# Kernel optimization log

Measured on AMD Instinct MI355X. Metric: run time of the kernel, lower is better.

## Reference

```python
import jax, jax.numpy as jnp
import numpy as np

N_JOINTS = 16
N_VERTS = 778
# standard MANO kinematic tree (parent of joint i; root parent is -1, unused)
PARENTS = np.array([-1, 0, 1, 2, 0, 4, 5, 0, 7, 8, 0, 10, 11, 0, 13, 14])
# rotate_base=True: root rotation is post-multiplied by 180-deg rotation about x
ROT_X = np.array([[1.0, 0.0, 0.0], [0.0, -1.0, 0.0], [0.0, 0.0, -1.0]], dtype=np.float32)


def _batch_rodrigues(theta):
    # theta: [M, 3] axis-angle -> [M, 3, 3] rotation matrices (via quaternion, HMR-style)
    angle = jnp.linalg.norm(theta + 1e-8, axis=1, keepdims=True)
    axis = theta / angle
    half = 0.5 * angle
    quat = jnp.concatenate([jnp.cos(half), jnp.sin(half) * axis], axis=1)
    quat = quat / jnp.linalg.norm(quat, axis=1, keepdims=True)
    w, x, y, z = quat[:, 0], quat[:, 1], quat[:, 2], quat[:, 3]
    w2, x2, y2, z2 = w * w, x * x, y * y, z * z
    wx, wy, wz = w * x, w * y, w * z
    xy, xz, yz = x * y, x * z, y * z
    R = jnp.stack([
        w2 + x2 - y2 - z2, 2 * xy - 2 * wz, 2 * wy + 2 * xz,
        2 * wz + 2 * xy, w2 - x2 + y2 - z2, 2 * yz - 2 * wx,
        2 * xz - 2 * wy, 2 * wx + 2 * yz, w2 - x2 - y2 + z2,
    ], axis=1)
    return R.reshape(-1, 3, 3)


def _make_A(R, t):
    # R: [N,3,3], t: [N,3] -> [N,4,4] homogeneous transform
    top = jnp.concatenate([R, t[:, :, None]], axis=2)          # [N,3,4]
    bot = jnp.broadcast_to(jnp.array([0.0, 0.0, 0.0, 1.0], R.dtype), (R.shape[0], 1, 4))
    return jnp.concatenate([top, bot], axis=1)


def _global_rigid_transform(Rs, J):
    # Rs: [N,16,3,3], J: [N,16,3]
    root_rotation = jnp.matmul(Rs[:, 0], jnp.asarray(ROT_X, Rs.dtype))
    results = [_make_A(root_rotation, J[:, 0])]
    for i in range(1, N_JOINTS):
        p = int(PARENTS[i])
        t = J[:, i] - J[:, p]
        results.append(jnp.matmul(results[p], _make_A(Rs[:, i], t)))
    G = jnp.stack(results, axis=1)                              # [N,16,4,4]
    J_transformed = G[:, :, :3, 3]
    # A = G - pad(G[:, :, :3, :3] @ J) : remove joint-rest translation
    rel = jnp.einsum('njab,njb->nja', G[:, :, :3, :3], J)       # [N,16,3]
    A = G.at[:, :, :3, 3].add(-rel)
    return J_transformed, A


def setup_inputs() -> dict:
    key = jax.random.key(0)
    ks = jax.random.split(key, 7)
    N = 4096
    return {
        'beta': jax.random.normal(ks[0], (N, 10), jnp.float32),
        'theta': jax.random.normal(ks[1], (N, 48), jnp.float32) * 0.3,
        'v_template': jax.random.normal(ks[2], (N_VERTS, 3), jnp.float32) * 0.1,
        'shapedirs': jax.random.normal(ks[3], (10, N_VERTS * 3), jnp.float32) * 0.01,
        'J_regressor': jax.random.uniform(ks[4], (N_VERTS, N_JOINTS), jnp.float32) / N_VERTS,
        'posedirs': jax.random.normal(ks[5], (135, N_VERTS * 3), jnp.float32) * 0.01,
        'weights': jax.random.uniform(ks[6], (N_VERTS, N_JOINTS), jnp.float32),
    }


def reference(beta, theta, v_template, shapedirs, J_regressor, posedirs, weights):
    N = beta.shape[0]
    # shape blendshapes
    v_shaped = jnp.matmul(beta, shapedirs).reshape(N, N_VERTS, 3) + v_template
    # rest joints from vertices
    J = jnp.einsum('nvc,vj->njc', v_shaped, J_regressor)        # [N,16,3]
    # pose rotations
    Rs = _batch_rodrigues(theta.reshape(-1, 3)).reshape(N, N_JOINTS, 3, 3)
    # pose blendshapes (exclude root)
    pose_feature = (Rs[:, 1:] - jnp.eye(3, dtype=Rs.dtype)).reshape(N, 135)
    v_posed = jnp.matmul(pose_feature, posedirs).reshape(N, N_VERTS, 3) + v_shaped
    # kinematic chain
    J_transformed, A = _global_rigid_transform(Rs, J)
    # linear blend skinning
    T = jnp.einsum('vj,njab->nvab', weights, A)                 # [N,778,4,4]
    ones = jnp.ones((N, N_VERTS, 1), v_posed.dtype)
    v_homo = jnp.concatenate([v_posed, ones], axis=2)           # [N,778,4]
    verts = jnp.einsum('nvab,nvb->nva', T, v_homo)[:, :, :3]    # [N,778,3]
    joints = jnp.einsum('nvc,vj->njc', verts, J_regressor)      # [N,16,3]
    return verts, joints, Rs
```

## Files before the change

kernel.cpp:

```cpp
#include <hip/hip_runtime.h>
#include <math.h>

#define NJ 16
#define NV 778
#define M3 2334
#define NTB 156

typedef float f32x4  __attribute__((ext_vector_type(4)));
typedef float f32x16 __attribute__((ext_vector_type(16)));
typedef short bf16x8 __attribute__((ext_vector_type(8)));

__device__ __forceinline__ unsigned short f2bf(float x) {
    unsigned int u = __float_as_uint(x);
    unsigned int r = (u + 0x7FFF + ((u >> 16) & 1)) >> 16;
    return (unsigned short)r;
}


__global__ __launch_bounds__(256, 1) void k01_prep(
    const float* __restrict__ shapedirs,
    const float* __restrict__ posedirs,
    const float* __restrict__ Jreg,
    const float* __restrict__ vtemp,
    const float* __restrict__ theta,
    float* __restrict__ SJJT,
    float* __restrict__ RsOut,
    bf16x8* __restrict__ Bf,
    int N)
{
    const int tid = threadIdx.x;
    const int rodBlocks = (N * NJ) / 256;
    if (blockIdx.x < 44) {
        int task = blockIdx.x * 4 + (tid >> 6);
        int lane = tid & 63;
        if (task < 176) {
            int b = task >> 4;
            int j = task & 15;
            const float* src = (b < 10) ? (shapedirs + (size_t)b * M3) : vtemp;
            float a0 = 0.f, a1 = 0.f, a2 = 0.f;
            for (int v = lane; v < NV; v += 64) {
                float jr = Jreg[v * 16 + j];
                a0 = fmaf(src[v*3 + 0], jr, a0);
                a1 = fmaf(src[v*3 + 1], jr, a1);
                a2 = fmaf(src[v*3 + 2], jr, a2);
            }
#pragma unroll
            for (int m = 1; m < 64; m <<= 1) {
                a0 += __shfl_xor(a0, m);
                a1 += __shfl_xor(a1, m);
                a2 += __shfl_xor(a2, m);
            }
            if (lane == 0) {
                int base = (b < 10) ? (b*48 + j*3) : (480 + j*3);
                SJJT[base + 0] = a0;
                SJJT[base + 1] = a1;
                SJJT[base + 2] = a2;
            }
        }
        return;
    }
    if (blockIdx.x < 44 + rodBlocks) {
        int idx = (blockIdx.x - 44) * 256 + tid;
        int n = idx >> 4;
        int j = idx & 15;
        float t0 = theta[n*48 + j*3 + 0];
        float t1 = theta[n*48 + j*3 + 1];
        float t2 = theta[n*48 + j*3 + 2];
        const float eps = 1e-8f;
        float a0 = t0 + eps, a1 = t1 + eps, a2 = t2 + eps;
        float angle = sqrtf(a0*a0 + a1*a1 + a2*a2);
        float inv  = 1.0f / angle;
        float half = 0.5f * angle;
        float sh = sinf(half), chh = cosf(half);
        float qw = chh;
        float qx = sh * t0 * inv;
        float qy = sh * t1 * inv;
        float qz = sh * t2 * inv;
        float qn = 1.0f / sqrtf(qw*qw + qx*qx + qy*qy + qz*qz);
        qw *= qn; qx *= qn; qy *= qn; qz *= qn;
        float w2=qw*qw, x2=qx*qx, y2=qy*qy, z2=qz*qz;
        float wx=qw*qx, wy=qw*qy, wz=qw*qz;
        float xy=qx*qy, xz=qx*qz, yz=qy*qz;
        float* R = RsOut + (size_t)idx * 9;
        R[0] = w2 + x2 - y2 - z2;
        R[1] = 2.f*(xy - wz);
        R[2] = 2.f*(wy + xz);
        R[3] = 2.f*(wz + xy);
        R[4] = w2 - x2 + y2 - z2;
        R[5] = 2.f*(yz - wx);
        R[6] = 2.f*(xz - wy);
        R[7] = 2.f*(wx + yz);
        R[8] = w2 - x2 - y2 + z2;
        return;
    }
    int idx = (blockIdx.x - 44 - rodBlocks) * 256 + tid;
    int nB = NTB * 5 * 64;
    if (idx >= nB) return;
    int lane = idx & 63;
    int ks   = (idx >> 6) % 5;
    int nt   = idx / 320;
    int col = nt * 16 + (lane & 15);
    int k0  = ks * 32 + (lane >> 4) * 8;
    bf16x8 o;
#pragma unroll
    for (int j = 0; j < 8; ++j) {
        int k = k0 + j;
        float val = 0.f;
        if (col < M3) {
            if (k < 10)       val = shapedirs[(size_t)k * M3 + col];
            else if (k < 145) val = posedirs[(size_t)(k - 10) * M3 + col];
        }
        o[j] = (short)f2bf(val);
    }
    Bf[idx] = o;
}

__global__ __launch_bounds__(256, 1) void k2m(
    const float* __restrict__ beta,
    const float* __restrict__ Rs,
    const float* __restrict__ SJJT,
    float* __restrict__ Aws,
    bf16x8* __restrict__ Af,
    int N)
{
    const int tid = threadIdx.x;
    const int KB2 = (N * 5 + 255) / 256;
    if (blockIdx.x < KB2) {
        __shared__ float sS[528];
        for (int i = tid; i < 528; i += 256) sS[i] = SJJT[i];
        __syncthreads();
        int gid = blockIdx.x * 256 + tid;
        if (gid >= N * 5) return;
        int n  = gid / 5;
        int ch = gid % 5;

        float b[10];
#pragma unroll
        for (int i = 0; i < 10; ++i) b[i] = beta[n*10 + i];

        int jidx[4];
        jidx[0] = 0; jidx[1] = ch*3 + 1; jidx[2] = ch*3 + 2; jidx[3] = ch*3 + 3;
        float J[4][3];
#pragma unroll
        for (int q = 0; q < 4; ++q) {
            int j = jidx[q];
#pragma unroll
            for (int c = 0; c < 3; ++c) {
                float acc = sS[480 + j*3 + c];
#pragma unroll
                for (int qq = 0; qq < 10; ++qq)
                    acc = fmaf(b[qq], sS[qq*48 + j*3 + c], acc);
                J[q][c] = acc;
            }
        }

        const float* Rn = Rs + (size_t)n * 144;
        float* An = Aws + (size_t)n * 192;

        float GpR[9], Gpt[3];
#pragma unroll
        for (int r = 0; r < 3; ++r) {
            GpR[r*3+0] =  Rn[r*3+0];
            GpR[r*3+1] = -Rn[r*3+1];
            GpR[r*3+2] = -Rn[r*3+2];
        }
        Gpt[0] = J[0][0]; Gpt[1] = J[0][1]; Gpt[2] = J[0][2];

        if (ch == 0) {
#pragma unroll
            for (int r = 0; r < 3; ++r) {
                float rel = GpR[r*3+0]*J[0][0] + GpR[r*3+1]*J[0][1] + GpR[r*3+2]*J[0][2];
                An[r*4 + 0] = GpR[r*3+0];
                An[r*4 + 1] = GpR[r*3+1];
                An[r*4 + 2] = GpR[r*3+2];
                An[r*4 + 3] = Gpt[r] - rel;
            }
        }

#pragma unroll
        for (int st = 0; st < 3; ++st) {
            int i = jidx[st+1];
            const float* Ri = Rn + (size_t)i * 9;
            float t0 = J[st+1][0] - J[st][0];
            float t1 = J[st+1][1] - J[st][1];
            float t2 = J[st+1][2] - J[st][2];
            float GR[9], Gt[3];
#pragma unroll
            for (int r = 0; r < 3; ++r) {
#pragma unroll
                for (int c = 0; c < 3; ++c)
                    GR[r*3+c] = GpR[r*3+0]*Ri[c] + GpR[r*3+1]*Ri[3+c] + GpR[r*3+2]*Ri[6+c];
                Gt[r] = GpR[r*3+0]*t0 + GpR[r*3+1]*t1 + GpR[r*3+2]*t2 + Gpt[r];
            }
#pragma unroll
            for (int r = 0; r < 3; ++r) {
                float rel = GR[r*3+0]*J[st+1][0] + GR[r*3+1]*J[st+1][1] + GR[r*3+2]*J[st+1][2];
                An[i*12 + r*4 + 0] = GR[r*3+0];
                An[i*12 + r*4 + 1] = GR[r*3+1];
                An[i*12 + r*4 + 2] = GR[r*3+2];
                An[i*12 + r*4 + 3] = Gt[r] - rel;
            }
#pragma unroll
            for (int r = 0; r < 9; ++r) GpR[r] = GR[r];
            Gpt[0] = Gt[0]; Gpt[1] = Gt[1]; Gpt[2] = Gt[2];
        }
        return;
    }

    int idx = (blockIdx.x - KB2) * 256 + tid;
    int nA = (N / 16) * 5 * 64;
    if (idx >= nA) return;
    int lane = idx & 63;
    int ks   = (idx >> 6) % 5;
    int mt   = idx / 320;
    int n  = mt * 16 + (lane & 15);
    int k0 = ks * 32 + (lane >> 4) * 8;
    bf16x8 o;
#pragma unroll
    for (int j = 0; j < 8; ++j) {
        int k = k0 + j;
        float val;
        if (k < 10) {
            val = beta[(size_t)n * 10 + k];
        } else if (k < 145) {
            int kk = k - 10;
            int rr = kk % 9;
            val = Rs[(size_t)n * 144 + 9 + kk];
            if ((rr & 3) == 0) val -= 1.f;
        } else {
            val = 0.f;
        }
        o[j] = (short)f2bf(val);
    }
    Af[idx] = o;
}

__global__ __launch_bounds__(256, 1) void k34_gemm_blend(
    const bf16x8* __restrict__ Af,
    const bf16x8* __restrict__ Bf,
    const float* __restrict__ vtemp,
    const float* __restrict__ Aws,
    const float* __restrict__ weights,
    float* __restrict__ verts,
    int N)
{
    __shared__ float sC[16][194];
    const int tid  = threadIdx.x;
    const int w    = tid >> 6;
    const int lane = tid & 63;
    const int mt   = blockIdx.x;
    const int ntb  = blockIdx.y * 12 + w * 3;

    f32x4 acc0 = {0.f,0.f,0.f,0.f};
    f32x4 acc1 = {0.f,0.f,0.f,0.f};
    f32x4 acc2 = {0.f,0.f,0.f,0.f};

    const bf16x8* Ab = Af + (size_t)mt * 5 * 64 + lane;
    const bf16x8* Bb = Bf + lane;

#pragma unroll
    for (int ks = 0; ks < 5; ++ks) {
        bf16x8 a  = Ab[ks * 64];
        bf16x8 b0 = Bb[((size_t)(ntb+0) * 5 + ks) * 64];
        bf16x8 b1 = Bb[((size_t)(ntb+1) * 5 + ks) * 64];
        bf16x8 b2 = Bb[((size_t)(ntb+2) * 5 + ks) * 64];
        acc0 = __builtin_amdgcn_mfma_f32_16x16x32_bf16(a, b0, acc0, 0, 0, 0);
        acc1 = __builtin_amdgcn_mfma_f32_16x16x32_bf16(a, b1, acc1, 0, 0, 0);
        acc2 = __builtin_amdgcn_mfma_f32_16x16x32_bf16(a, b2, acc2, 0, 0, 0);
    }

    {
        const int rl = (lane >> 4) * 4;
        const int cl = w * 48 + (lane & 15);
#pragma unroll
        for (int r = 0; r < 4; ++r) {
            sC[rl + r][cl +  0] = acc0[r];
            sC[rl + r][cl + 16] = acc1[r];
            sC[rl + r][cl + 32] = acc2[r];
        }
    }
    __syncthreads();

    const int vg = blockIdx.y * 64 + lane;
    const bool valid = vg < NV;
    const int cvg = valid ? vg : (NV - 1);

    f32x16 wv = *reinterpret_cast<const f32x16*>(&weights[(size_t)cvg * 16]);
    float vtx = vtemp[cvg*3 + 0];
    float vty = vtemp[cvg*3 + 1];
    float vtz = vtemp[cvg*3 + 2];

#pragma unroll
    for (int it = 0; it < 4; ++it) {
        const int nl = w * 4 + it;
        const int n  = __builtin_amdgcn_readfirstlane(mt * 16 + nl);
        const float* An = Aws + (size_t)n * 192;

        float px = sC[nl][lane*3 + 0] + vtx;
        float py = sC[nl][lane*3 + 1] + vty;
        float pz = sC[nl][lane*3 + 2] + vtz;

        float ox = 0.f, oy = 0.f, oz = 0.f;
#define BJF(j_) { \
        float a0=An[(j_)*12+0],  a1=An[(j_)*12+1],  a2 =An[(j_)*12+2],  a3 =An[(j_)*12+3]; \
        float a4=An[(j_)*12+4],  a5=An[(j_)*12+5],  a6 =An[(j_)*12+6],  a7 =An[(j_)*12+7]; \
        float a8=An[(j_)*12+8],  a9=An[(j_)*12+9],  a10=An[(j_)*12+10], a11=An[(j_)*12+11]; \
        float X = fmaf(a0,px, fmaf(a1,py, fmaf(a2,pz, a3))); \
        float Y = fmaf(a4,px, fmaf(a5,py, fmaf(a6,pz, a7))); \
        float Z = fmaf(a8,px, fmaf(a9,py, fmaf(a10,pz, a11))); \
        ox = fmaf(wv[j_], X, ox); oy = fmaf(wv[j_], Y, oy); oz = fmaf(wv[j_], Z, oz); }
        BJF(0)  BJF(1)  BJF(2)  BJF(3)  BJF(4)  BJF(5)  BJF(6)  BJF(7)
        BJF(8)  BJF(9)  BJF(10) BJF(11) BJF(12) BJF(13) BJF(14) BJF(15)
#undef BJF

        if (valid) {
            float* o = verts + (size_t)(mt*16 + nl) * M3 + (size_t)vg * 3;
            o[0] = ox; o[1] = oy; o[2] = oz;
        }
    }
}

__global__ __launch_bounds__(256, 1) void k4b_joints(
    const float* __restrict__ verts,
    const float* __restrict__ Jreg,
    float* __restrict__ joints,
    int N)
{
    __shared__ float part[4][4][48];
    const int tid = threadIdx.x;
    const int nl  = tid >> 6;
    const int sub = tid & 63;
    const int j   = sub & 15;
    const int c4  = sub >> 4;
    const int n   = blockIdx.x * 4 + nl;

    int vbeg = c4 * 195;
    int vend = vbeg + 195; if (vend > NV) vend = NV;

    const float* vp = verts + (size_t)n * M3;
    float a0 = 0.f, a1 = 0.f, a2 = 0.f;
#pragma unroll 4
    for (int v = vbeg; v < vend; ++v) {
        float jr = Jreg[(size_t)v * 16 + j];
        float x = vp[v*3 + 0], y = vp[v*3 + 1], z = vp[v*3 + 2];
        a0 = fmaf(jr, x, a0);
        a1 = fmaf(jr, y, a1);
        a2 = fmaf(jr, z, a2);
    }
    part[nl][c4][j*3+0] = a0;
    part[nl][c4][j*3+1] = a1;
    part[nl][c4][j*3+2] = a2;
    __syncthreads();

    if (tid < 192) {
        int nl2 = tid / 48;
        int r   = tid % 48;
        float s = part[nl2][0][r] + part[nl2][1][r] + part[nl2][2][r] + part[nl2][3][r];
        joints[(size_t)(blockIdx.x * 4 + nl2) * 48 + r] = s;
    }
}

extern "C" void kernel_launch(void* const* d_in, const int* in_sizes, int n_in,
                              void* d_out, int out_size, void* d_ws, size_t ws_size,
                              hipStream_t stream)
{
    const float* beta   = (const float*)d_in[0];
    const float* theta  = (const float*)d_in[1];
    const float* vtemp  = (const float*)d_in[2];
    const float* shaped = (const float*)d_in[3];
    const float* Jreg   = (const float*)d_in[4];
    const float* posed  = (const float*)d_in[5];
    const float* wts    = (const float*)d_in[6];
    float* out = (float*)d_out;
    const int N = in_sizes[0] / 10;

    float* verts  = out;
    float* joints = out + (size_t)N * M3;
    float* RsOut  = joints + (size_t)N * 48;
    float* Aws    = (float*)d_ws;
    float*  fbase = Aws + (size_t)N * 192;
    bf16x8* Af    = (bf16x8*)fbase;
    bf16x8* Bf    = (bf16x8*)(fbase + (size_t)(N/16)*5*64*4);

    const int nA = (N / 16) * 5 * 64;
    const int nB = NTB * 5 * 64;
    const int rodBlocks = (N * NJ) / 256;
    const int KB2 = (N * 5 + 255) / 256;

    k01_prep<<<44 + rodBlocks + (nB + 255)/256, 256, 0, stream>>>(
        shaped, posed, Jreg, vtemp, theta, joints, RsOut, Bf, N);
    k2m<<<KB2 + (nA + 255)/256, 256, 0, stream>>>(
        beta, RsOut, joints, Aws, Af, N);
    k34_gemm_blend<<<dim3(N/16, 13), 256, 0, stream>>>(
        Af, Bf, vtemp, Aws, wts, verts, N);
    k4b_joints<<<N/4, 256, 0, stream>>>(verts, Jreg, joints, N);
}
```

Before: 82.20 us.

## Fold k2m into prep and GEMM kernels, recomputing Rodrigues for A-fragment packing

Removes the separate k2m launch. The bf16 A-fragment packing moves into the prep kernel, which recomputes the Rodrigues rotations from theta instead of waiting for the Rs output. The per-sample kinematic chain moves into the start of the GEMM/blend kernel, where 80 threads per block compute the transforms into the workspace. This saves a launch and a global round-trip for A, but every y-block redundantly recomputes the chain for its 16 samples and delays the MFMA work until it finishes.

```diff
diff --git a/kernel.cpp b/kernel.cpp
--- a/kernel.cpp
+++ b/kernel.cpp
@@ -14,6 +14,37 @@
     unsigned int u = __float_as_uint(x);
     unsigned int r = (u + 0x7FFF + ((u >> 16) & 1)) >> 16;
     return (unsigned short)r;
+}
+
+__device__ __forceinline__ void rodrigues9(
+    float t0, float t1, float t2,
+    float& r0, float& r1, float& r2, float& r3, float& r4,
+    float& r5, float& r6, float& r7, float& r8)
+{
+    const float eps = 1e-8f;
+    float a0 = t0 + eps, a1 = t1 + eps, a2 = t2 + eps;
+    float angle = sqrtf(a0*a0 + a1*a1 + a2*a2);
+    float inv  = 1.0f / angle;
+    float half = 0.5f * angle;
+    float sh = sinf(half), chh = cosf(half);
+    float qw = chh;
+    float qx = sh * t0 * inv;
+    float qy = sh * t1 * inv;
+    float qz = sh * t2 * inv;
+    float qn = 1.0f / sqrtf(qw*qw + qx*qx + qy*qy + qz*qz);
+    qw *= qn; qx *= qn; qy *= qn; qz *= qn;
+    float w2=qw*qw, x2=qx*qx, y2=qy*qy, z2=qz*qz;
+    float wx=qw*qx, wy=qw*qy, wz=qw*qz;
+    float xy=qx*qy, xz=qx*qz, yz=qy*qz;
+    r0 = w2 + x2 - y2 - z2;
+    r1 = 2.f*(xy - wz);
+    r2 = 2.f*(wy + xz);
+    r3 = 2.f*(wz + xy);
+    r4 = w2 - x2 + y2 - z2;
+    r5 = 2.f*(yz - wx);
+    r6 = 2.f*(xz - wy);
+    r7 = 2.f*(wx + yz);
+    r8 = w2 - x2 - y2 + z2;
 }
 
 
@@ -23,13 +54,17 @@
     const float* __restrict__ Jreg,
     const float* __restrict__ vtemp,
     const float* __restrict__ theta,
+    const float* __restrict__ beta,
     float* __restrict__ SJJT,
     float* __restrict__ RsOut,
     bf16x8* __restrict__ Bf,
+    bf16x8* __restrict__ Af,
     int N)
 {
     const int tid = threadIdx.x;
     const int rodBlocks = (N * NJ) / 256;
+    const int nB = NTB * 5 * 64;
+    const int bfBlocks = nB / 256;
     if (blockIdx.x < 44) {
         int task = blockIdx.x * 4 + (tid >> 6);
         int lane = tid & 63;
@@ -63,76 +98,109 @@
         int idx = (blockIdx.x - 44) * 256 + tid;
         int n = idx >> 4;
         int j = idx & 15;
-        float t0 = theta[n*48 + j*3 + 0];
-        float t1 = theta[n*48 + j*3 + 1];
-        float t2 = theta[n*48 + j*3 + 2];
-        const float eps = 1e-8f;
-        float a0 = t0 + eps, a1 = t1 + eps, a2 = t2 + eps;
-        float angle = sqrtf(a0*a0 + a1*a1 + a2*a2);
-        float inv  = 1.0f / angle;
-        float half = 0.5f * angle;
-        float sh = sinf(half), chh = cosf(half);
-        float qw = chh;
-        float qx = sh * t0 * inv;
-        float qy = sh * t1 * inv;
-        float qz = sh * t2 * inv;
-        float qn = 1.0f / sqrtf(qw*qw + qx*qx + qy*qy + qz*qz);
-        qw *= qn; qx *= qn; qy *= qn; qz *= qn;
-        float w2=qw*qw, x2=qx*qx, y2=qy*qy, z2=qz*qz;
-        float wx=qw*qx, wy=qw*qy, wz=qw*qz;
-        float xy=qx*qy, xz=qx*qz, yz=qy*qz;
+        float r0,r1,r2,r3,r4,r5,r6,r7,r8;
+        rodrigues9(theta[n*48 + j*3 + 0], theta[n*48 + j*3 + 1],
+                   theta[n*48 + j*3 + 2], r0,r1,r2,r3,r4,r5,r6,r7,r8);
         float* R = RsOut + (size_t)idx * 9;
-        R[0] = w2 + x2 - y2 - z2;
-        R[1] = 2.f*(xy - wz);
-        R[2] = 2.f*(wy + xz);
-        R[3] = 2.f*(wz + xy);
-        R[4] = w2 - x2 + y2 - z2;
-        R[5] = 2.f*(yz - wx);
-        R[6] = 2.f*(xz - wy);
-        R[7] = 2.f*(wx + yz);
-        R[8] = w2 - x2 - y2 + z2;
+        R[0]=r0; R[1]=r1; R[2]=r2; R[3]=r3; R[4]=r4;
+        R[5]=r5; R[6]=r6; R[7]=r7; R[8]=r8;
         return;
     }
-    int idx = (blockIdx.x - 44 - rodBlocks) * 256 + tid;
-    int nB = NTB * 5 * 64;
-    if (idx >= nB) return;
+    if (blockIdx.x < 44 + rodBlocks + bfBlocks) {
+        int idx = (blockIdx.x - 44 - rodBlocks) * 256 + tid;
+        int lane = idx & 63;
+        int ks   = (idx >> 6) % 5;
+        int nt   = idx / 320;
+        int col = nt * 16 + (lane & 15);
+        int k0  = ks * 32 + (lane >> 4) * 8;
+        bf16x8 o;
+#pragma unroll
+        for (int j = 0; j < 8; ++j) {
+            int k = k0 + j;
+            float val = 0.f;
+            if (col < M3) {
+                if (k < 10)       val = shapedirs[(size_t)k * M3 + col];
+                else if (k < 145) val = posedirs[(size_t)(k - 10) * M3 + col];
+            }
+            o[j] = (short)f2bf(val);
+        }
+        Bf[idx] = o;
+        return;
+    }
+    int idx = (blockIdx.x - 44 - rodBlocks - bfBlocks) * 256 + tid;
+    int nA = (N / 16) * 5 * 64;
+    if (idx >= nA) return;
     int lane = idx & 63;
     int ks   = (idx >> 6) % 5;
-    int nt   = idx / 320;
-    int col = nt * 16 + (lane & 15);
-    int k0  = ks * 32 + (lane >> 4) * 8;
+    int mt   = idx / 320;
+    int n  = mt * 16 + (lane & 15);
+    int k0 = ks * 32 + (lane >> 4) * 8;
+
+    int kkA = k0 - 10;
+    int jA  = (kkA < 0) ? 0 : (kkA > 134 ? 14 : kkA / 9);
+    int kkB = k0 - 3;
+    int jB  = (kkB < 0) ? 0 : (kkB > 134 ? 14 : kkB / 9);
+
+    float ra0,ra1,ra2,ra3,ra4,ra5,ra6,ra7,ra8;
+    rodrigues9(theta[n*48 + (jA+1)*3 + 0], theta[n*48 + (jA+1)*3 + 1],
+               theta[n*48 + (jA+1)*3 + 2], ra0,ra1,ra2,ra3,ra4,ra5,ra6,ra7,ra8);
+    float rb0,rb1,rb2,rb3,rb4,rb5,rb6,rb7,rb8;
+    rodrigues9(theta[n*48 + (jB+1)*3 + 0], theta[n*48 + (jB+1)*3 + 1],
+               theta[n*48 + (jB+1)*3 + 2], rb0,rb1,rb2,rb3,rb4,rb5,rb6,rb7,rb8);
+
     bf16x8 o;
 #pragma unroll
     for (int j = 0; j < 8; ++j) {
         int k = k0 + j;
-        float val = 0.f;
-        if (col < M3) {
-            if (k < 10)       val = shapedirs[(size_t)k * M3 + col];
-            else if (k < 145) val = posedirs[(size_t)(k - 10) * M3 + col];
+        float val;
+        if (k < 10) {
+            val = beta[(size_t)n * 10 + k];
+        } else if (k < 145) {
+            int kk = k - 10;
+            int jj = kk / 9;
+            int rr = kk - jj * 9;
+            float sa = (rr==0)?ra0:(rr==1)?ra1:(rr==2)?ra2:(rr==3)?ra3:
+                       (rr==4)?ra4:(rr==5)?ra5:(rr==6)?ra6:(rr==7)?ra7:ra8;
+            float sb = (rr==0)?rb0:(rr==1)?rb1:(rr==2)?rb2:(rr==3)?rb3:
+                       (rr==4)?rb4:(rr==5)?rb5:(rr==6)?rb6:(rr==7)?rb7:rb8;
+            float vv = (jj == jA) ? sa : sb;
+            if ((rr & 3) == 0) vv -= 1.f;
+            val = vv;
+        } else {
+            val = 0.f;
         }
         o[j] = (short)f2bf(val);
     }
-    Bf[idx] = o;
-}
-
-__global__ __launch_bounds__(256, 1) void k2m(
+    Af[idx] = o;
+}
+
+__global__ __launch_bounds__(256, 1) void k34_gemm_blend(
     const float* __restrict__ beta,
     const float* __restrict__ Rs,
-    const float* __restrict__ SJJT,
+    const bf16x8* __restrict__ Af,
+    const bf16x8* __restrict__ Bf,
+    const float* __restrict__ vtemp,
+    const float* __restrict__ weights,
+    const float* __restrict__ SJJTg,
     float* __restrict__ Aws,
-    bf16x8* __restrict__ Af,
+    float* __restrict__ verts,
     int N)
 {
-    const int tid = threadIdx.x;
-    const int KB2 = (N * 5 + 255) / 256;
-    if (blockIdx.x < KB2) {
-        __shared__ float sS[528];
-        for (int i = tid; i < 528; i += 256) sS[i] = SJJT[i];
-        __syncthreads();
-        int gid = blockIdx.x * 256 + tid;
-        if (gid >= N * 5) return;
-        int n  = gid / 5;
-        int ch = gid % 5;
+    __shared__ float sC[16][194];
+    __shared__ float sS[528];
+    const int tid  = threadIdx.x;
+    const int w    = tid >> 6;
+    const int lane = tid & 63;
+    const int mt   = blockIdx.x;
+    const int ntb  = blockIdx.y * 12 + w * 3;
+
+    for (int i = tid; i < 528; i += 256) sS[i] = SJJTg[i];
+    __syncthreads();
+
+    if (tid < 80) {
+        int n_loc = tid / 5;
+        int ch    = tid % 5;
+        int n     = mt * 16 + n_loc;
 
         float b[10];
 #pragma unroll
@@ -204,52 +272,7 @@
             for (int r = 0; r < 9; ++r) GpR[r] = GR[r];
             Gpt[0] = Gt[0]; Gpt[1] = Gt[1]; Gpt[2] = Gt[2];
         }
-        return;
-    }
-
-    int idx = (blockIdx.x - KB2) * 256 + tid;
-    int nA = (N / 16) * 5 * 64;
-    if (idx >= nA) return;
-    int lane = idx & 63;
-    int ks   = (idx >> 6) % 5;
-    int mt   = idx / 320;
-    int n  = mt * 16 + (lane & 15);
-    int k0 = ks * 32 + (lane >> 4) * 8;
-    bf16x8 o;
-#pragma unroll
-    for (int j = 0; j < 8; ++j) {
-        int k = k0 + j;
-        float val;
-        if (k < 10) {
-            val = beta[(size_t)n * 10 + k];
-        } else if (k < 145) {
-            int kk = k - 10;
-            int rr = kk % 9;
-            val = Rs[(size_t)n * 144 + 9 + kk];
-            if ((rr & 3) == 0) val -= 1.f;
-        } else {
-            val = 0.f;
-        }
-        o[j] = (short)f2bf(val);
-    }
-    Af[idx] = o;
-}
-
-__global__ __launch_bounds__(256, 1) void k34_gemm_blend(
-    const bf16x8* __restrict__ Af,
-    const bf16x8* __restrict__ Bf,
-    const float* __restrict__ vtemp,
-    const float* __restrict__ Aws,
-    const float* __restrict__ weights,
-    float* __restrict__ verts,
-    int N)
-{
-    __shared__ float sC[16][194];
-    const int tid  = threadIdx.x;
-    const int w    = tid >> 6;
-    const int lane = tid & 63;
-    const int mt   = blockIdx.x;
-    const int ntb  = blockIdx.y * 12 + w * 3;
+    }
 
     f32x4 acc0 = {0.f,0.f,0.f,0.f};
     f32x4 acc1 = {0.f,0.f,0.f,0.f};
@@ -385,13 +408,10 @@
     const int nA = (N / 16) * 5 * 64;
     const int nB = NTB * 5 * 64;
     const int rodBlocks = (N * NJ) / 256;
-    const int KB2 = (N * 5 + 255) / 256;
-
-    k01_prep<<<44 + rodBlocks + (nB + 255)/256, 256, 0, stream>>>(
-        shaped, posed, Jreg, vtemp, theta, joints, RsOut, Bf, N);
-    k2m<<<KB2 + (nA + 255)/256, 256, 0, stream>>>(
-        beta, RsOut, joints, Aws, Af, N);
+
+    k01_prep<<<44 + rodBlocks + nB/256 + nA/256, 256, 0, stream>>>(
+        shaped, posed, Jreg, vtemp, theta, beta, joints, RsOut, Bf, Af, N);
     k34_gemm_blend<<<dim3(N/16, 13), 256, 0, stream>>>(
-        Af, Bf, vtemp, Aws, wts, verts, N);
+        beta, RsOut, Af, Bf, vtemp, wts, joints, Aws, verts, N);
     k4b_joints<<<N/4, 256, 0, stream>>>(verts, Jreg, joints, N);
 }
```

Measured after the change: 149.4 us. +81.8%, slower.
